# Performance work log

Measured on AMD Instinct MI355X. Metric: run time of the kernel, lower is better.

Reference implementation:

```python
import jax, jax.numpy as jnp
import numpy as np

N, E, G = 50000, 800000, 64
IN, H, C = 128, 3, 64
HC = H * C


def _conv(x, src, dst, Wq, bq, Wk, bk, Wv, bv, Ws, bs, Wb):
    # node-level projections, then per-edge gather
    q = (x @ Wq + bq).reshape(-1, H, C)[dst]   # [E,H,C]
    k = (x @ Wk + bk).reshape(-1, H, C)[src]
    v = (x @ Wv + bv).reshape(-1, H, C)[src]
    alpha = (q * k).sum(-1) / jnp.sqrt(jnp.float32(C))  # [E,H]
    # segment softmax over incoming edges of each target node
    amax = jax.ops.segment_max(alpha, dst, num_segments=N)
    amax = jnp.where(jnp.isfinite(amax), amax, 0.0)
    ex = jnp.exp(alpha - amax[dst])
    denom = jax.ops.segment_sum(ex, dst, num_segments=N)
    a = ex / (denom[dst] + 1e-16)
    out = jax.ops.segment_sum(a[:, :, None] * v, dst, num_segments=N).reshape(-1, HC)
    # gated skip (beta=True, root_weight=True)
    r = x @ Ws + bs
    beta = jax.nn.sigmoid(jnp.concatenate([out, r, out - r], -1) @ Wb)  # [N,1]
    return beta * r + (1.0 - beta) * out


def setup_inputs() -> dict:
    key = jax.random.key(0)
    ks = jax.random.split(key, 32)
    x = jax.random.normal(ks[0], (N, IN), dtype=jnp.float32)
    edge_index = jax.random.randint(ks[1], (2, E), 0, N, dtype=jnp.int32)
    batch = jnp.sort(jax.random.randint(ks[2], (N,), 0, G, dtype=jnp.int32))
    s = 0.05
    def w(k, shape):
        return jax.random.normal(k, shape, dtype=jnp.float32) * s
    d = {"x": x, "edge_index": edge_index, "batch": batch}
    ins = [IN, HC]
    ki = 3
    for l in range(2):
        din = ins[l]
        d[f"Wq{l}"] = w(ks[ki], (din, HC)); ki += 1
        d[f"bq{l}"] = jnp.zeros((HC,), jnp.float32)
        d[f"Wk{l}"] = w(ks[ki], (din, HC)); ki += 1
        d[f"bk{l}"] = jnp.zeros((HC,), jnp.float32)
        d[f"Wv{l}"] = w(ks[ki], (din, HC)); ki += 1
        d[f"bv{l}"] = jnp.zeros((HC,), jnp.float32)
        d[f"Ws{l}"] = w(ks[ki], (din, HC)); ki += 1
        d[f"bs{l}"] = jnp.zeros((HC,), jnp.float32)
        d[f"Wb{l}"] = w(ks[ki], (3 * HC, 1)); ki += 1
    d["Wlin"] = w(ks[ki], (HC, 1)); ki += 1
    d["blin"] = jnp.zeros((1,), jnp.float32)
    return d


def reference(x, edge_index, batch,
              Wq0, bq0, Wk0, bk0, Wv0, bv0, Ws0, bs0, Wb0,
              Wq1, bq1, Wk1, bk1, Wv1, bv1, Ws1, bs1, Wb1,
              Wlin, blin):
    src, dst = edge_index[0], edge_index[1]
    h = _conv(x, src, dst, Wq0, bq0, Wk0, bk0, Wv0, bv0, Ws0, bs0, Wb0)
    h = jax.nn.elu(h)
    h = _conv(h, src, dst, Wq1, bq1, Wk1, bk1, Wv1, bv1, Ws1, bs1, Wb1)
    h = jax.nn.elu(h)
    # global mean pool over graphs
    cnt = jax.ops.segment_sum(jnp.ones((N,), jnp.float32), batch, num_segments=G)
    pooled = jax.ops.segment_sum(h, batch, num_segments=G) / jnp.maximum(cnt, 1.0)[:, None]
    logits = (pooled @ Wlin + blin).squeeze(-1)  # [G]
    return logits
```

## Files before the change

kernel.cpp:

```cpp
#include <hip/hip_runtime.h>
#include <math.h>

#define NNODES 50000
#define NEDGES 800000
#define NGRAPH 64
#define DIM_IN 128
#define HCDIM  192
#define QKVRW  768

typedef __attribute__((ext_vector_type(8))) short short8;
typedef __attribute__((ext_vector_type(4))) float f32x4;
typedef __attribute__((ext_vector_type(2))) float f32x2;

__device__ __forceinline__ unsigned short f2bf(float f){
  unsigned int u = __float_as_uint(f);
  unsigned int r = (u + 0x7fffu + ((u>>16)&1u)) >> 16;
  return (unsigned short)r;
}

__device__ __forceinline__ f32x2 bf2_to_f2(unsigned int u){
  f32x2 r;
  r[0] = __uint_as_float(u<<16);
  r[1] = __uint_as_float(u & 0xffff0000u);
  return r;
}

__device__ __forceinline__ f32x2 fp8_lo(unsigned int u){
  return __builtin_amdgcn_cvt_pk_f32_fp8((int)u, false);
}
__device__ __forceinline__ f32x2 fp8_hi(unsigned int u){
  return __builtin_amdgcn_cvt_pk_f32_fp8((int)u, true);
}

__device__ __forceinline__ float wave_sum(float v){
#pragma unroll
  for(int off=32; off>0; off>>=1) v += __shfl_xor(v, off, 64);
  return v;
}

__global__ void hist_k(const int* __restrict__ dst, int* __restrict__ counts, int E){
  int e = blockIdx.x*blockDim.x + threadIdx.x;
  if(e<E) atomicAdd(&counts[dst[e]], 1);
}

__global__ void scan_partial(const int* __restrict__ counts, int* __restrict__ bsum, int N){
  __shared__ int lds[256];
  int t = threadIdx.x;
  int idx = blockIdx.x*256 + t;
  int v = (idx<N)? counts[idx] : 0;
  lds[t]=v; __syncthreads();
#pragma unroll
  for(int off=128; off>0; off>>=1){
    if(t<off) lds[t]+=lds[t+off];
    __syncthreads();
  }
  if(t==0) bsum[blockIdx.x]=lds[0];
}

__global__ void scan_bsum(int* bsum, int nb){
  __shared__ int lds[1024];
  int t=threadIdx.x;
  int v=(t<nb)?bsum[t]:0;
  lds[t]=v; __syncthreads();
  int x=v;
#pragma unroll
  for(int off=1; off<1024; off<<=1){
    int y=(t>=off)?lds[t-off]:0;
    __syncthreads();
    x+=y; lds[t]=x;
    __syncthreads();
  }
  if(t<nb) bsum[t]=x-v;
}

__global__ void scan_final(const int* __restrict__ counts, const int* __restrict__ bsum,
                           int* __restrict__ row_ptr, int N){
  __shared__ int lds[256];
  int t=threadIdx.x;
  int idx=blockIdx.x*256+t;
  int v=(idx<N)?counts[idx]:0;
  lds[t]=v; __syncthreads();
  int x=v;
#pragma unroll
  for(int off=1; off<256; off<<=1){
    int y=(t>=off)?lds[t-off]:0;
    __syncthreads();
    x+=y; lds[t]=x;
    __syncthreads();
  }
  if(idx<=N) row_ptr[idx]= bsum[blockIdx.x]+x-v;
}

__global__ void fill_k(const int* __restrict__ src, const int* __restrict__ dst,
                       const int* __restrict__ row_ptr, int* __restrict__ cursor,
                       int* __restrict__ csr_src, int E){
  int e = blockIdx.x*blockDim.x + threadIdx.x;
  if(e<E){
    int d = dst[e];
    int pos = row_ptr[d] + atomicAdd(&cursor[d], 1);
    csr_src[pos] = src[e];
  }
}

#define CAST_BLKS (NNODES*DIM_IN/4/256)
#define WT0_BLKS  ((QKVRW*DIM_IN+255)/256)
#define WT1_BLKS  ((QKVRW*HCDIM+255)/256)
__global__ void prep_all(const float* __restrict__ X, unsigned short* __restrict__ Xb,
  const float* __restrict__ Wq0,const float* __restrict__ Wk0,
  const float* __restrict__ Wv0,const float* __restrict__ Ws0,
  const float* __restrict__ bq0,const float* __restrict__ bk0,
  const float* __restrict__ bv0,const float* __restrict__ bs0,
  unsigned short* __restrict__ Wt0, float* __restrict__ bcat0,
  const float* __restrict__ Wq1,const float* __restrict__ Wk1,
  const float* __restrict__ Wv1,const float* __restrict__ Ws1,
  const float* __restrict__ bq1,const float* __restrict__ bk1,
  const float* __restrict__ bv1,const float* __restrict__ bs1,
  unsigned short* __restrict__ Wt1, float* __restrict__ bcat1)
{
  const int b = blockIdx.x;
  if(b < CAST_BLKS){
    int i4 = (b*256 + threadIdx.x)*4;
    float4 v = *(const float4*)(X+i4);
    ushort4 o; o.x=f2bf(v.x); o.y=f2bf(v.y); o.z=f2bf(v.z); o.w=f2bf(v.w);
    *(ushort4*)(Xb+i4) = o;
  } else if(b < CAST_BLKS+WT0_BLKS){
    int idx = (b-CAST_BLKS)*256 + threadIdx.x;
    if(idx < QKVRW*DIM_IN){
      int c = idx / DIM_IN, k = idx % DIM_IN;
      int mat = c/HCDIM, cm = c%HCDIM;
      const float* W = (mat==0)?Wq0:(mat==1)?Ws0:(mat==2)?Wk0:Wv0;
      Wt0[(size_t)c*DIM_IN + k] = f2bf(W[(size_t)k*HCDIM + cm]);
    }
    if(idx < QKVRW){
      int mat = idx/HCDIM, cm = idx%HCDIM;
      const float* bb = (mat==0)?bq0:(mat==1)?bs0:(mat==2)?bk0:bv0;
      bcat0[idx] = bb[cm];
    }
  } else {
    int idx = (b-CAST_BLKS-WT0_BLKS)*256 + threadIdx.x;
    if(idx < QKVRW*HCDIM){
      int c = idx / HCDIM, k = idx % HCDIM;
      int mat = c/HCDIM, cm = c%HCDIM;
      const float* W = (mat==0)?Wq1:(mat==1)?Ws1:(mat==2)?Wk1:Wv1;
      Wt1[(size_t)c*HCDIM + k] = f2bf(W[(size_t)k*HCDIM + cm]);
    }
    if(idx < QKVRW){
      int mat = idx/HCDIM, cm = idx%HCDIM;
      const float* bb = (mat==0)?bq1:(mat==1)?bs1:(mat==2)?bk1:bv1;
      bcat1[idx] = bb[cm];
    }
  }
}

template<int K>
__global__ __launch_bounds__(256) void gemm_mfma(
    const unsigned short* __restrict__ Xb,
    const unsigned short* __restrict__ Wt,
    const float* __restrict__ bcat,
    unsigned short* __restrict__ QR,
    unsigned char* __restrict__ KV, int N)
{
  __shared__ unsigned short As[128*64];
  __shared__ unsigned short Bs[128*64];
  const int tid = threadIdx.x;
  const int wv = tid>>6;
  const int lane = tid&63;
  const int m0  = blockIdx.x*128;
  const int nc0 = blockIdx.y*128;

  const int wr = wv>>1, wc = wv&1;
  const int lhi = lane>>4, llo = lane&15;
  f32x4 acc[4][4] = {};

  constexpr int NT = K/64;
#pragma unroll
  for(int kt=0; kt<NT; ++kt){
    if(kt>0) __syncthreads();
#pragma unroll
    for(int it=0; it<4; ++it){
      int p = it*256 + tid;
      int r = p>>3, c = p&7;
      int cs = c ^ (r&7);
      int grow = m0 + r; if(grow > N-1) grow = N-1;
      const unsigned short* gp = Xb + (size_t)grow*K + kt*64 + cs*8;
      unsigned short* lp = As + (size_t)(it*256 + wv*64)*8;
      __builtin_amdgcn_global_load_lds(
          (const __attribute__((address_space(1))) unsigned int*)gp,
          (__attribute__((address_space(3))) unsigned int*)lp, 16, 0, 0);
    }
#pragma unroll
    for(int it=0; it<4; ++it){
      int p = it*256 + tid;
      int r = p>>3, c = p&7;
      int cs = c ^ (r&7);
      const unsigned short* gp = Wt + (size_t)(nc0 + r)*K + kt*64 + cs*8;
      unsigned short* lp = Bs + (size_t)(it*256 + wv*64)*8;
      __builtin_amdgcn_global_load_lds(
          (const __attribute__((address_space(1))) unsigned int*)gp,
          (__attribute__((address_space(3))) unsigned int*)lp, 16, 0, 0);
    }
    __syncthreads();

#pragma unroll
    for(int kk=0; kk<64; kk+=32){
      short8 a[4], b[4];
      const int chunk = (kk>>3) + lhi;
#pragma unroll
      for(int i=0;i<4;++i){
        int rr = wr*64 + i*16 + llo;
        int cs = chunk ^ (rr&7);
        a[i] = *(const short8*)(As + rr*64 + cs*8);
      }
#pragma unroll
      for(int j=0;j<4;++j){
        int cc = wc*64 + j*16 + llo;
        int cs = chunk ^ (cc&7);
        b[j] = *(const short8*)(Bs + cc*64 + cs*8);
      }
#pragma unroll
      for(int i=0;i<4;++i)
#pragma unroll
        for(int j=0;j<4;++j)
          acc[i][j] = __builtin_amdgcn_mfma_f32_16x16x32_bf16(a[i], b[j], acc[i][j], 0,0,0);
    }
  }

  if(nc0 < 384){
#pragma unroll
    for(int j=0;j<4;++j){
      const int col = nc0 + wc*64 + j*16 + llo;
      const float bias = bcat[col];
#pragma unroll
      for(int i=0;i<4;++i){
#pragma unroll
        for(int r=0;r<4;++r){
          int grow = m0 + wr*64 + i*16 + lhi*4 + r;
          if(grow < N) QR[(size_t)grow*384 + col] = f2bf(acc[i][j][r] + bias);
        }
      }
    }
  } else {
#pragma unroll
    for(int j=0;j<4;++j){
      const int col = nc0 - 384 + wc*64 + j*16 + llo;
      const float bias = bcat[col + 384];
#pragma unroll
      for(int i=0;i<4;++i){
#pragma unroll
        for(int r=0;r<4;++r){
          int grow = m0 + wr*64 + i*16 + lhi*4 + r;
          float v0 = acc[i][j][r] + bias;
          float n0 = __shfl_xor(v0, 1, 64);
          if(((llo&1)==0) && grow < N){
            int p0 = __builtin_amdgcn_cvt_pk_fp8_f32(v0, n0, 0, false);
            *(unsigned short*)(KV + (size_t)grow*384 + col) = (unsigned short)(p0 & 0xffff);
          }
        }
      }
    }
  }
}

template<bool OUTBF>
__global__ __launch_bounds__(256) void attn_kernel(
  const unsigned short* __restrict__ QR,
  const unsigned char* __restrict__ KV,
  const int* __restrict__ row_ptr, const int* __restrict__ csr_src,
  const float* __restrict__ Wb, float* __restrict__ HoutF,
  unsigned short* __restrict__ HoutB, int N)
{
  const int wave = threadIdx.x>>6;
  const int lane = threadIdx.x&63;
  const int g    = lane>>4;
  const int l    = lane&15;
  const int n = blockIdx.x*4 + wave;
  if(n>=N) return;

  const unsigned short* nr = QR + (size_t)n*384 + 4*l;
  f32x2 qlo[3], qhi[3];
#pragma unroll
  for(int h=0;h<3;++h){
    uint2 u = *(const uint2*)(nr + 64*h);
    qlo[h] = bf2_to_f2(u.x) * 0.125f;
    qhi[h] = bf2_to_f2(u.y) * 0.125f;
  }

  const int s0 = row_ptr[n];
  const int deg = row_ptr[n+1]-s0;

  f32x2 aLo[3] = {{0,0},{0,0},{0,0}};
  f32x2 aHi[3] = {{0,0},{0,0},{0,0}};
  float d0=0.f,d1=0.f,d2=0.f;

  unsigned int ku0=0,ku1=0,ku2=0,vu0=0,vu1=0,vu2=0;
  if(deg>0){
    int i0 = s0 + (g<deg ? g : 0); if(i0 > NEDGES-1) i0 = NEDGES-1;
    int sCur = csr_src[i0];
    const unsigned int* kv = (const unsigned int*)(KV + (size_t)sCur*384) + l;
    ku0=kv[0]; ku1=kv[16]; ku2=kv[32]; vu0=kv[48]; vu1=kv[64]; vu2=kv[80];
  }
  for(int base=0; base<deg; base+=4){
    const int inext = base + 4 + g;
    const int sNxt = csr_src[s0 + (inext<deg ? inext : 0)];
    const unsigned int* kvN = (const unsigned int*)(KV + (size_t)sNxt*384) + l;
    unsigned int nk0=kvN[0], nk1=kvN[16], nk2=kvN[32];
    unsigned int nv0=kvN[48], nv1=kvN[64], nv2=kvN[80];

    const bool valid = (base + g < deg);
    f32x2 t0 = qlo[0]*fp8_lo(ku0) + qhi[0]*fp8_hi(ku0);
    f32x2 t1 = qlo[1]*fp8_lo(ku1) + qhi[1]*fp8_hi(ku1);
    f32x2 t2 = qlo[2]*fp8_lo(ku2) + qhi[2]*fp8_hi(ku2);
    float p0 = t0[0]+t0[1];
    float p1 = t1[0]+t1[1];
    float p2 = t2[0]+t2[1];
#pragma unroll
    for(int off=1; off<16; off<<=1){
      p0 += __shfl_xor(p0, off, 64);
      p1 += __shfl_xor(p1, off, 64);
      p2 += __shfl_xor(p2, off, 64);
    }
    float e0 = valid ? __expf(p0) : 0.f;
    float e1 = valid ? __expf(p1) : 0.f;
    float e2 = valid ? __expf(p2) : 0.f;
    d0 += e0; d1 += e1; d2 += e2;
    f32x2 e20 = {e0,e0}, e21 = {e1,e1}, e22 = {e2,e2};
    aLo[0] = fp8_lo(vu0)*e20 + aLo[0];
    aHi[0] = fp8_hi(vu0)*e20 + aHi[0];
    aLo[1] = fp8_lo(vu1)*e21 + aLo[1];
    aHi[1] = fp8_hi(vu1)*e21 + aHi[1];
    aLo[2] = fp8_lo(vu2)*e22 + aLo[2];
    aHi[2] = fp8_hi(vu2)*e22 + aHi[2];

    ku0=nk0; ku1=nk1; ku2=nk2; vu0=nv0; vu1=nv1; vu2=nv2;
  }

#pragma unroll
  for(int off=16; off<64; off<<=1){
#pragma unroll
    for(int h=0;h<3;++h){
      aLo[h][0]+=__shfl_xor(aLo[h][0],off,64); aLo[h][1]+=__shfl_xor(aLo[h][1],off,64);
      aHi[h][0]+=__shfl_xor(aHi[h][0],off,64); aHi[h][1]+=__shfl_xor(aHi[h][1],off,64);
    }
    d0+=__shfl_xor(d0,off,64); d1+=__shfl_xor(d1,off,64); d2+=__shfl_xor(d2,off,64);
  }
  const float dsum[3] = {d0,d1,d2};
  f32x2 oLo[3], oHi[3], rLo[3], rHi[3];
#pragma unroll
  for(int h=0;h<3;++h){
    float inv = 1.f/(dsum[h]+1e-16f);
    oLo[h] = aLo[h]*inv; oHi[h] = aHi[h]*inv;
    uint2 ur = *(const uint2*)(nr + 192 + 64*h);
    rLo[h] = bf2_to_f2(ur.x); rHi[h] = bf2_to_f2(ur.y);
  }

  f32x2 zz = {0,0};
#pragma unroll
  for(int h=0;h<3;++h){
    const float* wO = Wb + 64*h + 4*l;
    const float* wR = Wb + 192 + 64*h + 4*l;
    const float* wD = Wb + 384 + 64*h + 4*l;
    f32x2 woL = *(const f32x2*)(wO), woH = *(const f32x2*)(wO+2);
    f32x2 wrL = *(const f32x2*)(wR), wrH = *(const f32x2*)(wR+2);
    f32x2 wdL = *(const f32x2*)(wD), wdH = *(const f32x2*)(wD+2);
    zz = oLo[h]*woL + zz;
    zz = oHi[h]*woH + zz;
    zz = rLo[h]*wrL + zz;
    zz = rHi[h]*wrH + zz;
    zz = (oLo[h]-rLo[h])*wdL + zz;
    zz = (oHi[h]-rHi[h])*wdH + zz;
  }
  float z = zz[0]+zz[1];
#pragma unroll
  for(int off=1; off<16; off<<=1) z += __shfl_xor(z, off, 64);
  const float beta = 1.f/(1.f+__expf(-z));

  if(g==0){
#pragma unroll
    for(int h=0;h<3;++h){
      f32x2 hL = (rLo[h]-oLo[h])*beta + oLo[h];
      f32x2 hH = (rHi[h]-oHi[h])*beta + oHi[h];
      hL[0]=(hL[0]>0.f)?hL[0]:expm1f(hL[0]); hL[1]=(hL[1]>0.f)?hL[1]:expm1f(hL[1]);
      hH[0]=(hH[0]>0.f)?hH[0]:expm1f(hH[0]); hH[1]=(hH[1]>0.f)?hH[1]:expm1f(hH[1]);
      if(OUTBF){
        unsigned short* hb = HoutB + (size_t)n*HCDIM + 64*h + 4*l;
        ushort4 u;
        u.x=f2bf(hL[0]); u.y=f2bf(hL[1]); u.z=f2bf(hH[0]); u.w=f2bf(hH[1]);
        *(ushort4*)(hb) = u;
      } else {
        float* ho = HoutF + (size_t)n*HCDIM + 64*h + 4*l;
        float4 f; f.x=hL[0]; f.y=hL[1]; f.z=hH[0]; f.w=hH[1];
        *(float4*)(ho) = f;
      }
    }
  }
}

__global__ void pool_k(const float* __restrict__ H, const int* __restrict__ batch,
                       float* __restrict__ pooled, int* __restrict__ cnt, int N){
  const int t = threadIdx.x;
  int start = blockIdx.x*256;
  int end = min(start+256, N);
  if(start>=N) return;
  int cur = batch[start];
  float acc = 0.f;
  int run = 0;
  for(int nn=start; nn<end; ++nn){
    int g = batch[nn];
    if(g!=cur){
      atomicAdd(&pooled[(size_t)cur*HCDIM+t], acc);
      if(t==0) atomicAdd(&cnt[cur], run);
      acc=0.f; run=0; cur=g;
    }
    acc += H[(size_t)nn*HCDIM+t];
    run++;
  }
  atomicAdd(&pooled[(size_t)cur*HCDIM+t], acc);
  if(t==0) atomicAdd(&cnt[cur], run);
}

__global__ void logits_k(const float* __restrict__ pooled, const int* __restrict__ cnt,
                         const float* __restrict__ Wlin, const float* __restrict__ blin,
                         float* __restrict__ out){
  const int g = blockIdx.x;
  const int lane = threadIdx.x;
  float c = fmaxf((float)cnt[g], 1.f);
  float s = 0.f;
#pragma unroll
  for(int j=0;j<3;++j){
    int col = j*64+lane;
    s += pooled[(size_t)g*HCDIM+col]/c * Wlin[col];
  }
  s = wave_sum(s);
  if(lane==0) out[g] = s + blin[0];
}

extern "C" void kernel_launch(void* const* d_in, const int* in_sizes, int n_in,
                              void* d_out, int out_size, void* d_ws, size_t ws_size,
                              hipStream_t stream)
{
  const int N=NNODES, E=NEDGES;
  const float* x     = (const float*)d_in[0];
  const int*   ei    = (const int*)d_in[1];
  const int*   batch = (const int*)d_in[2];
  const int* esrc = ei;
  const int* edst = ei + E;
  const float* Wq0=(const float*)d_in[3];  const float* bq0=(const float*)d_in[4];
  const float* Wk0=(const float*)d_in[5];  const float* bk0=(const float*)d_in[6];
  const float* Wv0=(const float*)d_in[7];  const float* bv0=(const float*)d_in[8];
  const float* Ws0=(const float*)d_in[9];  const float* bs0=(const float*)d_in[10];
  const float* Wb0=(const float*)d_in[11];
  const float* Wq1=(const float*)d_in[12]; const float* bq1=(const float*)d_in[13];
  const float* Wk1=(const float*)d_in[14]; const float* bk1=(const float*)d_in[15];
  const float* Wv1=(const float*)d_in[16]; const float* bv1=(const float*)d_in[17];
  const float* Ws1=(const float*)d_in[18]; const float* bs1=(const float*)d_in[19];
  const float* Wb1=(const float*)d_in[20];
  const float* Wlin=(const float*)d_in[21];
  const float* blin=(const float*)d_in[22];
  float* out = (float*)d_out;

  char* p = (char*)d_ws;
  auto alloc = [&](size_t bytes)->char*{
    char* q = p; p += (bytes+255)/256*256; return q;
  };
  unsigned short* Xb   = (unsigned short*)alloc((size_t)N*HCDIM*2);
  unsigned short* QR   = (unsigned short*)alloc((size_t)N*384*2);
  unsigned char*  KV   = (unsigned char*)alloc((size_t)N*384);
  float* H1            = (float*)alloc((size_t)N*HCDIM*4);
  unsigned short* Wt0  = (unsigned short*)alloc((size_t)QKVRW*DIM_IN*2);
  float* bcat0         = (float*)alloc(QKVRW*4);
  unsigned short* Wt1  = (unsigned short*)alloc((size_t)QKVRW*HCDIM*2);
  float* bcat1         = (float*)alloc(QKVRW*4);
  const size_t CSR_CHUNK = ((size_t)N*4+255)/256*256;
  int* counts  = (int*)alloc(CSR_CHUNK);
  int* cursor  = (int*)alloc(CSR_CHUNK);
  int* row_ptr = (int*)alloc((size_t)(N+1)*4);
  int* csr     = (int*)alloc((size_t)E*4);
  int* bsum    = (int*)alloc(4096);
  float* pooled= (float*)alloc((size_t)NGRAPH*HCDIM*4);
  int* cnt     = (int*)alloc(256);

  const int NB = (N+255)/256;

  hipMemsetAsync(counts, 0, 2*CSR_CHUNK, stream);
  hipMemsetAsync(pooled, 0, (size_t)NGRAPH*HCDIM*4 + 256, stream);

  prep_all<<<CAST_BLKS + WT0_BLKS + WT1_BLKS, 256, 0, stream>>>(
      x, Xb,
      Wq0,Wk0,Wv0,Ws0, bq0,bk0,bv0,bs0, Wt0, bcat0,
      Wq1,Wk1,Wv1,Ws1, bq1,bk1,bv1,bs1, Wt1, bcat1);

  hist_k<<<(E+255)/256,256,0,stream>>>(edst,counts,E);
  scan_partial<<<NB,256,0,stream>>>(counts,bsum,N);
  scan_bsum<<<1,1024,0,stream>>>(bsum,NB);
  scan_final<<<NB,256,0,stream>>>(counts,bsum,row_ptr,N);
  fill_k<<<(E+255)/256,256,0,stream>>>(esrc,edst,row_ptr,cursor,csr,E);

  dim3 ggemm((N+127)/128, 6);
  gemm_mfma<DIM_IN><<<ggemm,256,0,stream>>>(Xb,Wt0,bcat0,QR,KV,N);
  attn_kernel<true><<<(N+3)/4,256,0,stream>>>(QR,KV,row_ptr,csr,Wb0,nullptr,Xb,N);
  gemm_mfma<HCDIM><<<ggemm,256,0,stream>>>(Xb,Wt1,bcat1,QR,KV,N);
  attn_kernel<false><<<(N+3)/4,256,0,stream>>>(QR,KV,row_ptr,csr,Wb1,H1,nullptr,N);

  pool_k<<<(N+255)/256,192,0,stream>>>(H1,batch,pooled,cnt,N);
  logits_k<<<NGRAPH,64,0,stream>>>(pooled,cnt,Wlin,blin,out);
}
```

Baseline: 408.9 us.

## Interleave K/V fp8 layout for 8-byte gathers and fuse histogram into prep kernel

The GEMM epilogue now writes K and V fp8 values interleaved per 4-column group, so each attention lane fetches K and V for a head with one 8-byte load instead of two 4-byte loads. This halves the number of gather instructions per edge in the memory-bound attention loop. Separately, the edge-destination histogram is folded into the prep_all launch as extra blocks, removing one kernel launch. The risk is that the epilogue's scattered 2-byte stores become less contiguous.

```diff
diff --git a/kernel.cpp b/kernel.cpp
--- a/kernel.cpp
+++ b/kernel.cpp
@@ -36,11 +36,6 @@
 #pragma unroll
   for(int off=32; off>0; off>>=1) v += __shfl_xor(v, off, 64);
   return v;
-}
-
-__global__ void hist_k(const int* __restrict__ dst, int* __restrict__ counts, int E){
-  int e = blockIdx.x*blockDim.x + threadIdx.x;
-  if(e<E) atomicAdd(&counts[dst[e]], 1);
 }
 
 __global__ void scan_partial(const int* __restrict__ counts, int* __restrict__ bsum, int N){
@@ -105,6 +100,7 @@
 #define CAST_BLKS (NNODES*DIM_IN/4/256)
 #define WT0_BLKS  ((QKVRW*DIM_IN+255)/256)
 #define WT1_BLKS  ((QKVRW*HCDIM+255)/256)
+#define HIST_BLKS ((NEDGES+255)/256)
 __global__ void prep_all(const float* __restrict__ X, unsigned short* __restrict__ Xb,
   const float* __restrict__ Wq0,const float* __restrict__ Wk0,
   const float* __restrict__ Wv0,const float* __restrict__ Ws0,
@@ -115,7 +111,8 @@
   const float* __restrict__ Wv1,const float* __restrict__ Ws1,
   const float* __restrict__ bq1,const float* __restrict__ bk1,
   const float* __restrict__ bv1,const float* __restrict__ bs1,
-  unsigned short* __restrict__ Wt1, float* __restrict__ bcat1)
+  unsigned short* __restrict__ Wt1, float* __restrict__ bcat1,
+  const int* __restrict__ edst, int* __restrict__ counts)
 {
   const int b = blockIdx.x;
   if(b < CAST_BLKS){
@@ -136,7 +133,7 @@
       const float* bb = (mat==0)?bq0:(mat==1)?bs0:(mat==2)?bk0:bv0;
       bcat0[idx] = bb[cm];
     }
-  } else {
+  } else if(b < CAST_BLKS+WT0_BLKS+WT1_BLKS){
     int idx = (b-CAST_BLKS-WT0_BLKS)*256 + threadIdx.x;
     if(idx < QKVRW*HCDIM){
       int c = idx / HCDIM, k = idx % HCDIM;
@@ -149,6 +146,9 @@
       const float* bb = (mat==0)?bq1:(mat==1)?bs1:(mat==2)?bk1:bv1;
       bcat1[idx] = bb[cm];
     }
+  } else {
+    int e = (b-CAST_BLKS-WT0_BLKS-WT1_BLKS)*256 + threadIdx.x;
+    if(e<NEDGES) atomicAdd(&counts[edst[e]], 1);
   }
 }
 
@@ -242,8 +242,15 @@
   } else {
 #pragma unroll
     for(int j=0;j<4;++j){
-      const int col = nc0 - 384 + wc*64 + j*16 + llo;
-      const float bias = bcat[col + 384];
+      const int c = nc0 - 384 + wc*64 + j*16 + llo;
+      const float bias = bcat[c + 384];
+      int off;
+      if(c < 192){
+        off = (c>>6)*128 + ((c&63)>>2)*8 + (c&3);
+      } else {
+        int c2 = c-192;
+        off = (c2>>6)*128 + ((c2&63)>>2)*8 + 4 + (c2&3);
+      }
 #pragma unroll
       for(int i=0;i<4;++i){
 #pragma unroll
@@ -253,7 +260,7 @@
           float n0 = __shfl_xor(v0, 1, 64);
           if(((llo&1)==0) && grow < N){
             int p0 = __builtin_amdgcn_cvt_pk_fp8_f32(v0, n0, 0, false);
-            *(unsigned short*)(KV + (size_t)grow*384 + col) = (unsigned short)(p0 & 0xffff);
+            *(unsigned short*)(KV + (size_t)grow*384 + off) = (unsigned short)(p0 & 0xffff);
           }
         }
       }
@@ -292,24 +299,27 @@
   f32x2 aHi[3] = {{0,0},{0,0},{0,0}};
   float d0=0.f,d1=0.f,d2=0.f;
 
-  unsigned int ku0=0,ku1=0,ku2=0,vu0=0,vu1=0,vu2=0;
+  uint2 kv0={0,0}, kv1={0,0}, kv2={0,0};
   if(deg>0){
     int i0 = s0 + (g<deg ? g : 0); if(i0 > NEDGES-1) i0 = NEDGES-1;
     int sCur = csr_src[i0];
-    const unsigned int* kv = (const unsigned int*)(KV + (size_t)sCur*384) + l;
-    ku0=kv[0]; ku1=kv[16]; ku2=kv[32]; vu0=kv[48]; vu1=kv[64]; vu2=kv[80];
+    const unsigned char* kb = KV + (size_t)sCur*384 + l*8;
+    kv0 = *(const uint2*)(kb);
+    kv1 = *(const uint2*)(kb+128);
+    kv2 = *(const uint2*)(kb+256);
   }
   for(int base=0; base<deg; base+=4){
     const int inext = base + 4 + g;
     const int sNxt = csr_src[s0 + (inext<deg ? inext : 0)];
-    const unsigned int* kvN = (const unsigned int*)(KV + (size_t)sNxt*384) + l;
-    unsigned int nk0=kvN[0], nk1=kvN[16], nk2=kvN[32];
-    unsigned int nv0=kvN[48], nv1=kvN[64], nv2=kvN[80];
+    const unsigned char* kbN = KV + (size_t)sNxt*384 + l*8;
+    uint2 n0 = *(const uint2*)(kbN);
+    uint2 n1 = *(const uint2*)(kbN+128);
+    uint2 n2 = *(const uint2*)(kbN+256);
 
     const bool valid = (base + g < deg);
-    f32x2 t0 = qlo[0]*fp8_lo(ku0) + qhi[0]*fp8_hi(ku0);
-    f32x2 t1 = qlo[1]*fp8_lo(ku1) + qhi[1]*fp8_hi(ku1);
-    f32x2 t2 = qlo[2]*fp8_lo(ku2) + qhi[2]*fp8_hi(ku2);
+    f32x2 t0 = qlo[0]*fp8_lo(kv0.x) + qhi[0]*fp8_hi(kv0.x);
+    f32x2 t1 = qlo[1]*fp8_lo(kv1.x) + qhi[1]*fp8_hi(kv1.x);
+    f32x2 t2 = qlo[2]*fp8_lo(kv2.x) + qhi[2]*fp8_hi(kv2.x);
     float p0 = t0[0]+t0[1];
     float p1 = t1[0]+t1[1];
     float p2 = t2[0]+t2[1];
@@ -324,14 +334,14 @@
     float e2 = valid ? __expf(p2) : 0.f;
     d0 += e0; d1 += e1; d2 += e2;
     f32x2 e20 = {e0,e0}, e21 = {e1,e1}, e22 = {e2,e2};
-    aLo[0] = fp8_lo(vu0)*e20 + aLo[0];
-    aHi[0] = fp8_hi(vu0)*e20 + aHi[0];
-    aLo[1] = fp8_lo(vu1)*e21 + aLo[1];
-    aHi[1] = fp8_hi(vu1)*e21 + aHi[1];
-    aLo[2] = fp8_lo(vu2)*e22 + aLo[2];
-    aHi[2] = fp8_hi(vu2)*e22 + aHi[2];
-
-    ku0=nk0; ku1=nk1; ku2=nk2; vu0=nv0; vu1=nv1; vu2=nv2;
+    aLo[0] = fp8_lo(kv0.y)*e20 + aLo[0];
+    aHi[0] = fp8_hi(kv0.y)*e20 + aHi[0];
+    aLo[1] = fp8_lo(kv1.y)*e21 + aLo[1];
+    aHi[1] = fp8_hi(kv1.y)*e21 + aHi[1];
+    aLo[2] = fp8_lo(kv2.y)*e22 + aLo[2];
+    aHi[2] = fp8_hi(kv2.y)*e22 + aHi[2];
+
+    kv0=n0; kv1=n1; kv2=n2;
   }
 
 #pragma unroll
@@ -484,12 +494,12 @@
   hipMemsetAsync(counts, 0, 2*CSR_CHUNK, stream);
   hipMemsetAsync(pooled, 0, (size_t)NGRAPH*HCDIM*4 + 256, stream);
 
-  prep_all<<<CAST_BLKS + WT0_BLKS + WT1_BLKS, 256, 0, stream>>>(
+  prep_all<<<CAST_BLKS + WT0_BLKS + WT1_BLKS + HIST_BLKS, 256, 0, stream>>>(
       x, Xb,
       Wq0,Wk0,Wv0,Ws0, bq0,bk0,bv0,bs0, Wt0, bcat0,
-      Wq1,Wk1,Wv1,Ws1, bq1,bk1,bv1,bs1, Wt1, bcat1);
-
-  hist_k<<<(E+255)/256,256,0,stream>>>(edst,counts,E);
+      Wq1,Wk1,Wv1,Ws1, bq1,bk1,bv1,bs1, Wt1, bcat1,
+      edst, counts);
+
   scan_partial<<<NB,256,0,stream>>>(counts,bsum,N);
   scan_bsum<<<1,1024,0,stream>>>(bsum,NB);
   scan_final<<<NB,256,0,stream>>>(counts,bsum,row_ptr,N);
```

New measurement: 419.4 us. 2.6% more time.
